# Kernel tuning notes

Hardware: AMD Instinct MI355X
Metric: run time of the kernel (lower is better)

The kernel has to match this reference:

```python
import jax, jax.numpy as jnp
import numpy as np

N = 40962      # icosahedral mesh nodes
E = 245760     # ~degree-6 mesh edges
HD = 256       # hidden_dim
H = 8          # heads
C = HD // H    # out_ch per head = 32
EDIM = 16      # raw edge feature dim
L = 4          # num_layers


def setup_inputs() -> dict:
    key = jax.random.key(0)
    ks = iter(jax.random.split(key, 48))
    def rn(shape, scale=0.05):
        return jax.random.normal(next(ks), shape, dtype=jnp.float32) * scale
    inp = {}
    inp['mesh_enc'] = jax.random.normal(next(ks), (N, HD), dtype=jnp.float32)
    inp['edge_index'] = jax.random.randint(next(ks), (2, E), 0, N)
    inp['edge_attr'] = jax.random.normal(next(ks), (E, EDIM), dtype=jnp.float32)
    # edge input projection
    inp['ep_W'] = rn((EDIM, HD)); inp['ep_b'] = jnp.zeros((HD,), jnp.float32)
    # GATv2 layer 0 (in_ch=HD) and layers 1..L-1 stacked (in_ch=C)
    inp['Wl0'] = rn((HD, H, C));  inp['Wr0'] = rn((HD, H, C))
    inp['Wl'] = rn((L - 1, C, H, C)); inp['Wr'] = rn((L - 1, C, H, C))
    inp['We0'] = rn((HD, H, C));  inp['We'] = rn((L - 1, HD, H, C))
    inp['att0'] = rn((H, C));     inp['att'] = rn((L - 1, H, C))
    inp['Wres0'] = rn((HD, C));   inp['Wres'] = rn((L - 1, C, C))
    inp['bn0'] = jnp.zeros((C,), jnp.float32); inp['bn'] = jnp.zeros((L - 1, C), jnp.float32)
    # edge-update MLP (upd_hidden_dim = hidden_dim * ffn_ratio = HD)
    inp['Wu1_0'] = rn((2 * C + HD, HD)); inp['Wu1'] = rn((L - 1, 2 * C + HD, HD))
    inp['bu1_0'] = jnp.zeros((HD,), jnp.float32); inp['bu1'] = jnp.zeros((L - 1, HD), jnp.float32)
    inp['Wu2_0'] = rn((HD, HD)); inp['Wu2'] = rn((L - 1, HD, HD))
    inp['bu2_0'] = jnp.zeros((HD,), jnp.float32); inp['bu2'] = jnp.zeros((L - 1, HD), jnp.float32)
    # inter-layer LayerNorms (L-1 of them, over C)
    inp['ln_g'] = jnp.ones((L - 1, C), jnp.float32); inp['ln_b'] = jnp.zeros((L - 1, C), jnp.float32)
    # SGFormer-style global branch
    inp['Wq'] = rn((HD, H, C)); inp['Wk'] = rn((HD, H, C)); inp['Wv'] = rn((HD, H, C))
    inp['alpha_p'] = jnp.array(0.5, jnp.float32)
    inp['cn_g'] = jnp.ones((C,), jnp.float32); inp['cn_b'] = jnp.zeros((C,), jnp.float32)
    return inp


def _layernorm(x, g, b):
    mu = x.mean(-1, keepdims=True)
    var = x.var(-1, keepdims=True)
    return (x - mu) / jnp.sqrt(var + 1e-5) * g + b


def _segment_softmax(s, dst, n):
    smax = jax.ops.segment_max(s, dst, num_segments=n)
    smax = jnp.where(jnp.isfinite(smax), smax, 0.0)
    ex = jnp.exp(s - smax[dst])
    den = jax.ops.segment_sum(ex, dst, num_segments=n)
    return ex / (den[dst] + 1e-16)


def _gat(x, e, src, dst, Wl, Wr, We, att, Wres, bn, Wu1, bu1, Wu2, bu2):
    # GATv2 with edge features (PyG semantics), concat=False (head mean), residual
    xl = jnp.einsum('nd,dhc->nhc', x, Wl)          # [N,H,C]
    xr = jnp.einsum('nd,dhc->nhc', x, Wr)
    ee = jnp.einsum('ed,dhc->ehc', e, We)          # [E,H,C]
    m = xl[src] + xr[dst] + ee
    s = jnp.einsum('ehc,hc->eh', jax.nn.leaky_relu(m, 0.2), att)
    a = _segment_softmax(s, dst, x.shape[0])       # [E,H]
    agg = jax.ops.segment_sum(a[:, :, None] * xl[src], dst, num_segments=x.shape[0])
    out = agg.mean(axis=1) + x @ Wres + bn         # [N,C]
    # residual edge update MLP
    h = jnp.concatenate([out[src], out[dst], e], axis=-1)
    e_new = e + jax.nn.gelu(h @ Wu1 + bu1) @ Wu2 + bu2
    return out, e_new


def _sgformer(x, Wq, Wk, Wv):
    # SGFormer linear global attention, O(N)
    q = jnp.einsum('nd,dhc->nhc', x, Wq)
    k = jnp.einsum('nd,dhc->nhc', x, Wk)
    v = jnp.einsum('nd,dhc->nhc', x, Wv)
    qs = q / (jnp.linalg.norm(q, axis=-1, keepdims=True) + 1e-6)
    ks = k / (jnp.linalg.norm(k, axis=-1, keepdims=True) + 1e-6)
    n = jnp.float32(x.shape[0])
    kv = jnp.einsum('nhc,nhd->hcd', ks, v)
    num = jnp.einsum('nhc,hcd->nhd', qs, kv) + n * v
    den = jnp.einsum('nhc,hc->nh', qs, ks.sum(0)) + n
    return (num / den[..., None]).mean(axis=1)     # [N,C]


def reference(mesh_enc, edge_index, edge_attr, ep_W, ep_b, Wl0, Wr0, Wl, Wr, We0, We,
              att0, att, Wres0, Wres, bn0, bn, Wu1_0, Wu1, bu1_0, bu1, Wu2_0, Wu2,
              bu2_0, bu2, ln_g, ln_b, Wq, Wk, Wv, alpha_p, cn_g, cn_b):
    src, dst = edge_index[0], edge_index[1]
    e = edge_attr @ ep_W + ep_b
    x, e = _gat(mesh_enc, e, src, dst, Wl0, Wr0, We0, att0, Wres0, bn0,
                Wu1_0, bu1_0, Wu2_0, bu2_0)
    x = _layernorm(x, ln_g[0], ln_b[0])
    for i in range(L - 1):
        x, e = _gat(x, e, src, dst, Wl[i], Wr[i], We[i], att[i], Wres[i], bn[i],
                    Wu1[i], bu1[i], Wu2[i], bu2[i])
        if i < L - 2:
            x = _layernorm(x, ln_g[i + 1], ln_b[i + 1])
    trans_out = _sgformer(mesh_enc, Wq, Wk, Wv)
    alpha = jax.nn.sigmoid(alpha_p)
    return _layernorm(alpha * x + (1.0 - alpha) * trans_out, cn_g, cn_b)
```

## Files before the change

kernel.cpp:

```cpp
#include <hip/hip_runtime.h>
#include <hip/hip_bf16.h>
#include <math.h>

typedef __hip_bfloat16 bf16;
typedef __attribute__((ext_vector_type(8))) __bf16 bf16x8;
typedef __attribute__((ext_vector_type(4))) float f32x4;

#define NN 40962
#define NE 245760
#define HDIM 256
#define NH 8
#define CH 32

#define MT 64
#define KVB 512

__device__ __forceinline__ float b2f(bf16 v) { return __bfloat162float(v); }
__device__ __forceinline__ bf16 f2b(float v) { return __float2bfloat16(v); }
__device__ __forceinline__ unsigned short f2bs(float v) {
  bf16 b = __float2bfloat16(v);
  return __builtin_bit_cast(unsigned short, b);
}
__device__ __forceinline__ float bs2f(unsigned short u) {
  return __bfloat162float(__builtin_bit_cast(bf16, u));
}

__device__ __forceinline__ float fast_gelu(float x) {
  float x2 = x * x;
  float g = x * (0.7978845608028654f + 0.0356774081f * x2);
  float y = fminf(g * 2.885390081777927f, 60.f);
  float t = exp2f(y);
  float th = (t - 1.f) * __builtin_amdgcn_rcpf(t + 1.f);
  return 0.5f * x * (1.f + th);
}

__global__ __launch_bounds__(512) void k_edge_proj_mfma(
    const float* __restrict__ attr, const unsigned short* __restrict__ Weps,
    const float* __restrict__ bias, bf16* __restrict__ e) {
  __shared__ unsigned short At[MT][40];
  __shared__ unsigned short O[MT][264];
  int tid = threadIdx.x, l = tid & 63, w = tid >> 6;
  int lr = l & 15, lk = l >> 4;
  int base = blockIdx.x * MT;
  {
    int p = tid >> 3, q = tid & 7;
    if (q < 4) {
      float4 v = *reinterpret_cast<const float4*>(&attr[(size_t)(base + p) * 16 + q * 4]);
      unsigned short tmp[4] = {f2bs(v.x), f2bs(v.y), f2bs(v.z), f2bs(v.w)};
      *reinterpret_cast<uint2*>(&At[p][q * 4]) = *reinterpret_cast<const uint2*>(tmp);
    } else {
      unsigned short z[4] = {0, 0, 0, 0};
      *reinterpret_cast<uint2*>(&At[p][q * 4]) = *reinterpret_cast<const uint2*>(z);
    }
  }
  __syncthreads();

  int j0 = w * 32;
  f32x4 acc[4][2];
#pragma unroll
  for (int m = 0; m < 4; ++m)
#pragma unroll
    for (int n = 0; n < 2; ++n)
#pragma unroll
      for (int r = 0; r < 4; ++r) acc[m][n][r] = 0.f;
  {
    bf16x8 a[4], b[2];
#pragma unroll
    for (int m = 0; m < 4; ++m)
      a[m] = *reinterpret_cast<const bf16x8*>(&At[m * 16 + lr][lk * 8]);
#pragma unroll
    for (int n = 0; n < 2; ++n) {
      int nt = w * 2 + n;
      b[n] = *reinterpret_cast<const bf16x8*>(Weps + ((size_t)nt * 64 + l) * 8);
    }
#pragma unroll
    for (int m = 0; m < 4; ++m)
#pragma unroll
      for (int n = 0; n < 2; ++n)
        acc[m][n] = __builtin_amdgcn_mfma_f32_16x16x32_bf16(a[m], b[n], acc[m][n], 0, 0, 0);
  }
#pragma unroll
  for (int n = 0; n < 2; ++n) {
    int col = j0 + n * 16 + lr;
    float bv = bias[col];
#pragma unroll
    for (int m = 0; m < 4; ++m)
#pragma unroll
      for (int r = 0; r < 4; ++r)
        O[m * 16 + lk * 4 + r][col] = f2bs(acc[m][n][r] + bv);
  }
  __syncthreads();
  for (int t = tid; t < MT * 32; t += 512) {
    int p = t >> 5, c = t & 31;
    *reinterpret_cast<uint4*>(&e[(size_t)(base + p) * HDIM + c * 8]) =
        *reinterpret_cast<const uint4*>(&O[p][c * 8]);
  }
}

__global__ void k_csr_count(const int* __restrict__ dst, int* __restrict__ cnt) {
  int e = blockIdx.x * 256 + threadIdx.x;
  if (e < NE) atomicAdd(&cnt[dst[e]], 1);
}
__global__ void k_csr_scan(const int* __restrict__ cnt, int* __restrict__ rowptr,
                           int* __restrict__ cursor) {
  __shared__ int part[256];
  __shared__ int tot;
  int t = threadIdx.x;
  const int CHUNK = (NN + 255) / 256;
  int lo = t * CHUNK, hi = lo + CHUNK; if (hi > NN) hi = NN; if (lo > NN) lo = NN;
  int s = 0;
  for (int i = lo; i < hi; ++i) s += cnt[i];
  part[t] = s;
  __syncthreads();
  if (t == 0) {
    int run = 0;
    for (int i = 0; i < 256; ++i) { int v = part[i]; part[i] = run; run += v; }
    tot = run;
  }
  __syncthreads();
  int run = part[t];
  for (int i = lo; i < hi; ++i) { rowptr[i] = run; cursor[i] = run; run += cnt[i]; }
  if (t == 0) rowptr[NN] = tot;
}
__global__ void k_csr_fill(const int* __restrict__ src, const int* __restrict__ dst,
                           int* __restrict__ cursor, int* __restrict__ csrsrc,
                           int* __restrict__ pos) {
  int e = blockIdx.x * 256 + threadIdx.x;
  if (e >= NE) return;
  int p = atomicAdd(&cursor[dst[e]], 1);
  csrsrc[p] = src[e];
  pos[e] = p;
}

struct SwzP {
  const float *We0, *WeL, *Wl0, *Wr0, *Wq, *Wk, *Wv;
  const float *Wu1_0, *Wu1L, *Wu2_0, *Wu2L, *WlL, *WrL, *epW;
  unsigned short *wall, *w1s, *w2s, *w32s, *wep;
  int* cnt;
};
__device__ __forceinline__ void swz1(const float* __restrict__ W,
                                     unsigned short* __restrict__ out, int t, int Kdiv32) {
  int i = t & 7, l = (t >> 3) & 63;
  int k0 = (t >> 9) % Kdiv32;
  int n0 = t / (512 * Kdiv32);
  int k = k0 * 32 + (l >> 4) * 8 + i;
  int n = n0 * 16 + (l & 15);
  out[t] = f2bs(W[k * 256 + n]);
}
#define SWZ_NW (9 * 65536)
#define SWZ_N1 (3 * 81920)
#define SWZ_N2 (3 * 65536)
#define SWZ_N3 (6 * 8192)
#define SWZ_N4 8192
__global__ void k_swz_fused(SwzP P) {
  int gid = blockIdx.x * 256 + threadIdx.x;
  if (gid < SWZ_NW) {
    int mat = gid >> 16, t = gid & 65535;
    const float* W;
    switch (mat) {
      case 0: W = P.We0; break;
      case 1: W = P.WeL; break;
      case 2: W = P.WeL + 65536; break;
      case 3: W = P.WeL + 131072; break;
      case 4: W = P.Wl0; break;
      case 5: W = P.Wr0; break;
      case 6: W = P.Wq; break;
      case 7: W = P.Wk; break;
      default: W = P.Wv; break;
    }
    swz1(W, P.wall + (size_t)mat * 65536, t, 8);
  } else if (gid < SWZ_NW + SWZ_N1) {
    int idx = gid - SWZ_NW;
    int mat = idx / 81920, t = idx % 81920;
    const float* W = (mat == 0) ? P.Wu1_0 : P.Wu1L + (size_t)(mat - 1) * 81920;
    swz1(W, P.w1s + (size_t)mat * 81920, t, 10);
  } else if (gid < SWZ_NW + SWZ_N1 + SWZ_N2) {
    int idx = gid - SWZ_NW - SWZ_N1;
    int mat = idx >> 16, t = idx & 65535;
    const float* W = (mat == 0) ? P.Wu2_0 : P.Wu2L + (size_t)(mat - 1) * 65536;
    swz1(W, P.w2s + (size_t)mat * 65536, t, 8);
  } else if (gid < SWZ_NW + SWZ_N1 + SWZ_N2 + SWZ_N3) {
    int idx = gid - SWZ_NW - SWZ_N1 - SWZ_N2;
    int mat = idx >> 13, t = idx & 8191;
    int i = mat >> 1;
    const float* W = (mat & 1) ? P.WrL + (size_t)i * 8192 : P.WlL + (size_t)i * 8192;
    swz1(W, P.w32s + (size_t)mat * 8192, t, 1);
  } else if (gid < SWZ_NW + SWZ_N1 + SWZ_N2 + SWZ_N3 + SWZ_N4) {
    int t = gid - (SWZ_NW + SWZ_N1 + SWZ_N2 + SWZ_N3);
    int i = t & 7, l = (t >> 3) & 63;
    int n0 = t >> 9;
    int k = (l >> 4) * 8 + i;
    int n = n0 * 16 + (l & 15);
    P.wep[t] = (k < 16) ? f2bs(P.epW[k * 256 + n]) : (unsigned short)0;
  } else {
    int i = gid - (SWZ_NW + SWZ_N1 + SWZ_N2 + SWZ_N3 + SWZ_N4);
    if (i < NN) P.cnt[i] = 0;
  }
}

__global__ __launch_bounds__(512) void k_edge_score_mfma(
    const bf16* __restrict__ e, const unsigned short* __restrict__ Wes,
    const bf16* __restrict__ xl, const bf16* __restrict__ xr,
    const float* __restrict__ att, const int* __restrict__ src,
    const int* __restrict__ dst, const int* __restrict__ pos,
    float* __restrict__ sxc) {
  __shared__ unsigned short Ae[MT][264];
  __shared__ float attS[HDIM];
  __shared__ int sidx[MT], didx[MT];
  int tid = threadIdx.x, l = tid & 63, w = tid >> 6;
  int lr = l & 15, lk = l >> 4;
  int base = blockIdx.x * MT;
  if (tid < HDIM) attS[tid] = att[tid];
  if (tid < MT) sidx[tid] = src[base + tid];
  else if (tid < 2 * MT) didx[tid - MT] = dst[base + tid - MT];
  for (int t = tid; t < MT * 32; t += 512) {
    int p = t >> 5, c = t & 31;
    *reinterpret_cast<uint4*>(&Ae[p][c * 8]) =
        *reinterpret_cast<const uint4*>(&e[(size_t)(base + p) * HDIM + c * 8]);
  }
  __syncthreads();

  f32x4 acc[4][2];
#pragma unroll
  for (int m = 0; m < 4; ++m)
#pragma unroll
    for (int n = 0; n < 2; ++n)
#pragma unroll
      for (int r = 0; r < 4; ++r) acc[m][n][r] = 0.f;
  for (int k0 = 0; k0 < 8; ++k0) {
    bf16x8 a[4], b[2];
#pragma unroll
    for (int m = 0; m < 4; ++m)
      a[m] = *reinterpret_cast<const bf16x8*>(&Ae[m * 16 + lr][k0 * 32 + lk * 8]);
#pragma unroll
    for (int n = 0; n < 2; ++n) {
      int nt = w * 2 + n;
      b[n] = *reinterpret_cast<const bf16x8*>(Wes + ((size_t)(nt * 8 + k0) * 64 + l) * 8);
    }
#pragma unroll
    for (int m = 0; m < 4; ++m)
#pragma unroll
      for (int n = 0; n < 2; ++n)
        acc[m][n] = __builtin_amdgcn_mfma_f32_16x16x32_bf16(a[m], b[n], acc[m][n], 0, 0, 0);
  }
  __syncthreads();

#pragma unroll
  for (int n = 0; n < 2; ++n) {
    int col = w * 32 + n * 16 + lr;
    float av = attS[col];
#pragma unroll
    for (int m = 0; m < 4; ++m)
#pragma unroll
      for (int r = 0; r < 4; ++r) {
        int row = m * 16 + lk * 4 + r;
        float xs = b2f(xl[(size_t)sidx[row] * HDIM + col]) +
                   b2f(xr[(size_t)didx[row] * HDIM + col]);
        float mm = acc[m][n][r] + xs;
        mm = (mm > 0.f) ? mm : 0.2f * mm;
        Ae[row][col] = f2bs(mm * av);
      }
  }
  __syncthreads();
  for (int pair = tid; pair < MT * NH; pair += 512) {
    int ed = pair >> 3, h = pair & 7;
    float s = 0.f;
#pragma unroll
    for (int c = 0; c < CH; ++c) s += bs2f(Ae[ed][h * CH + c]);
    sxc[(size_t)pos[base + ed] * NH + h] = expf(s);
  }
}

#define GCHUNK 64
template <int ID, bool LN>
__global__ __launch_bounds__(256) void k_gat_out(
    const int* __restrict__ rowptr, const int* __restrict__ csrsrc,
    const float* __restrict__ sxc, const bf16* __restrict__ xl,
    const float* __restrict__ x, const float* __restrict__ Wres,
    const float* __restrict__ bn, const float* __restrict__ lng,
    const float* __restrict__ lnb, float* __restrict__ xpre,
    float* __restrict__ xpost) {
  int n = blockIdx.x;
  int j = threadIdx.x;
  int h = j >> 5, c = j & 31;
  int p0 = rowptr[n], p1 = rowptr[n + 1];
  __shared__ int srcS[GCHUNK];
  __shared__ float exS[GCHUNK * NH];
  float a = 0.f, dsum = 0.f;
  for (int pb = p0; pb < p1; pb += GCHUNK) {
    int chunk = p1 - pb; if (chunk > GCHUNK) chunk = GCHUNK;
    if (j < chunk) srcS[j] = csrsrc[pb + j];
    for (int t = j; t < chunk * NH; t += 256) exS[t] = sxc[(size_t)pb * NH + t];
    __syncthreads();
    int i = 0;
    for (; i + 4 <= chunk; i += 4) {
      float e0 = exS[(i + 0) * NH + h], e1 = exS[(i + 1) * NH + h];
      float e2 = exS[(i + 2) * NH + h], e3 = exS[(i + 3) * NH + h];
      float x0 = b2f(xl[(size_t)srcS[i + 0] * HDIM + j]);
      float x1 = b2f(xl[(size_t)srcS[i + 1] * HDIM + j]);
      float x2 = b2f(xl[(size_t)srcS[i + 2] * HDIM + j]);
      float x3 = b2f(xl[(size_t)srcS[i + 3] * HDIM + j]);
      a += e0 * x0 + e1 * x1 + e2 * x2 + e3 * x3;
      dsum += e0 + e1 + e2 + e3;
    }
    for (; i < chunk; ++i) {
      float ev = exS[i * NH + h];
      a += ev * b2f(xl[(size_t)srcS[i] * HDIM + j]);
      dsum += ev;
    }
    __syncthreads();
  }
  __shared__ float oh[HDIM];
  __shared__ float rs[NH][CH];
  __shared__ float oc[CH + 1];
  oh[j] = a / (dsum + 1e-16f);
  const int KS = ID / NH;
  float r = 0.f;
  for (int k = h * KS; k < (h + 1) * KS; ++k)
    r += x[(size_t)n * ID + k] * Wres[k * CH + c];
  rs[h][c] = r;
  __syncthreads();
  if (j < CH) {
    float o = 0.f;
#pragma unroll
    for (int hh = 0; hh < NH; ++hh) o += oh[hh * CH + j];
    o *= (1.f / NH);
    float rr = 0.f;
#pragma unroll
    for (int hh = 0; hh < NH; ++hh) rr += rs[hh][j];
    o += rr + bn[j];
    xpre[(size_t)n * CH + j] = o;
    oc[j] = o;
  }
  __syncthreads();
  if (LN && j < CH) {
    float mu = 0.f;
#pragma unroll
    for (int k = 0; k < CH; ++k) mu += oc[k];
    mu *= (1.f / CH);
    float var = 0.f;
#pragma unroll
    for (int k = 0; k < CH; ++k) { float d = oc[k] - mu; var += d * d; }
    var *= (1.f / CH);
    xpost[(size_t)n * CH + j] = (oc[j] - mu) * rsqrtf(var + 1e-5f) * lng[j] + lnb[j];
  }
}

__global__ __launch_bounds__(512) void k_edge_mlp_mfma(
    bf16* __restrict__ e, const float* __restrict__ xo,
    const int* __restrict__ src, const int* __restrict__ dst,
    const unsigned short* __restrict__ W1s, const float* __restrict__ bu1,
    const unsigned short* __restrict__ W2s, const float* __restrict__ bu2) {
  __shared__ unsigned short buf[MT][328];
  __shared__ int sidx[MT], didx[MT];
  int tid = threadIdx.x;
  int l = tid & 63;
  int w = tid >> 6;
  int base = blockIdx.x * MT;
  int lr = l & 15;
  int lk = l >> 4;

  if (tid < MT) sidx[tid] = src[base + tid];
  else if (tid < 2 * MT) didx[tid - MT] = dst[base + tid - MT];
  __syncthreads();

  for (int t = tid; t < MT * 32; t += 512) {
    int p = t >> 5, cc = t & 31;
    uint4 v = *reinterpret_cast<const uint4*>(&e[(size_t)(base + p) * HDIM + cc * 8]);
    *reinterpret_cast<uint4*>(&buf[p][64 + cc * 8]) = v;
  }
  for (int t = tid; t < MT * 64; t += 512) {
    int p = t >> 6, c = t & 63;
    float v = (c < CH) ? xo[(size_t)sidx[p] * CH + c]
                       : xo[(size_t)didx[p] * CH + (c - CH)];
    buf[p][c] = f2bs(v);
  }
  __syncthreads();

  int j0 = w * 32;

  f32x4 acc[4][2];
#pragma unroll
  for (int m = 0; m < 4; ++m)
#pragma unroll
    for (int n = 0; n < 2; ++n)
#pragma unroll
      for (int r = 0; r < 4; ++r) acc[m][n][r] = 0.f;

  for (int k0 = 0; k0 < 10; ++k0) {
    bf16x8 a[4], b[2];
#pragma unroll
    for (int m = 0; m < 4; ++m)
      a[m] = *reinterpret_cast<const bf16x8*>(&buf[m * 16 + lr][k0 * 32 + lk * 8]);
#pragma unroll
    for (int n = 0; n < 2; ++n) {
      int nt = w * 2 + n;
      b[n] = *reinterpret_cast<const bf16x8*>(W1s + ((size_t)(nt * 10 + k0) * 64 + l) * 8);
    }
#pragma unroll
    for (int m = 0; m < 4; ++m)
#pragma unroll
      for (int n = 0; n < 2; ++n)
        acc[m][n] = __builtin_amdgcn_mfma_f32_16x16x32_bf16(a[m], b[n], acc[m][n], 0, 0, 0);
  }
  __syncthreads();

#pragma unroll
  for (int n = 0; n < 2; ++n) {
    float bv = bu1[j0 + n * 16 + lr];
#pragma unroll
    for (int m = 0; m < 4; ++m)
#pragma unroll
      for (int r = 0; r < 4; ++r) {
        float g = fast_gelu(acc[m][n][r] + bv);
        buf[m * 16 + lk * 4 + r][j0 + n * 16 + lr] = f2bs(g);
      }
  }
  __syncthreads();

#pragma unroll
  for (int m = 0; m < 4; ++m)
#pragma unroll
    for (int n = 0; n < 2; ++n)
#pragma unroll
      for (int r = 0; r < 4; ++r) acc[m][n][r] = 0.f;

  for (int k0 = 0; k0 < 8; ++k0) {
    bf16x8 a[4], b[2];
#pragma unroll
    for (int m = 0; m < 4; ++m)
      a[m] = *reinterpret_cast<const bf16x8*>(&buf[m * 16 + lr][k0 * 32 + lk * 8]);
#pragma unroll
    for (int n = 0; n < 2; ++n) {
      int nt = w * 2 + n;
      b[n] = *reinterpret_cast<const bf16x8*>(W2s + ((size_t)(nt * 8 + k0) * 64 + l) * 8);
    }
#pragma unroll
    for (int m = 0; m < 4; ++m)
#pragma unroll
      for (int n = 0; n < 2; ++n)
        acc[m][n] = __builtin_amdgcn_mfma_f32_16x16x32_bf16(a[m], b[n], acc[m][n], 0, 0, 0);
  }
  __syncthreads();

#pragma unroll
  for (int n = 0; n < 2; ++n) {
    int col = j0 + n * 16 + lr;
    float bv = bu2[col];
#pragma unroll
    for (int m = 0; m < 4; ++m)
#pragma unroll
      for (int r = 0; r < 4; ++r)
        buf[m * 16 + lk * 4 + r][col] = f2bs(acc[m][n][r] + bv);
  }
  __syncthreads();

  for (int t = tid; t < MT * 32; t += 512) {
    int p = t >> 5, cc = t & 31;
    uint4 dv = *reinterpret_cast<const uint4*>(&buf[p][cc * 8]);
    uint4 ev = *reinterpret_cast<const uint4*>(&e[(size_t)(base + p) * HDIM + cc * 8]);
    const unsigned short* dd = (const unsigned short*)&dv;
    const unsigned short* ee = (const unsigned short*)&ev;
    unsigned short ov[8];
#pragma unroll
    for (int i = 0; i < 8; ++i) ov[i] = f2bs(bs2f(ee[i]) + bs2f(dd[i]));
    *reinterpret_cast<uint4*>(&e[(size_t)(base + p) * HDIM + cc * 8]) =
        *reinterpret_cast<const uint4*>(ov);
  }
}

__global__ __launch_bounds__(256) void k_node_proj0_mfma(
    const float* __restrict__ x, const unsigned short* __restrict__ Wls,
    const unsigned short* __restrict__ Wrs, bf16* __restrict__ xl,
    bf16* __restrict__ xr) {
  __shared__ unsigned short A[MT][264];
  __shared__ unsigned short O[MT][264];
  int tid = threadIdx.x, l = tid & 63, w = tid >> 6;
  int lr = l & 15, lk = l >> 4;
  int base = blockIdx.x * MT;
  for (int t = tid; t < MT * 64; t += 256) {
    int p = t >> 6, c = t & 63;
    int row = base + p; if (row >= NN) row = NN - 1;
    float4 v = *reinterpret_cast<const float4*>(&x[(size_t)row * HDIM + c * 4]);
    unsigned short tmp[4] = {f2bs(v.x), f2bs(v.y), f2bs(v.z), f2bs(v.w)};
    *reinterpret_cast<uint2*>(&A[p][c * 4]) = *reinterpret_cast<const uint2*>(tmp);
  }
  __syncthreads();
  int j0 = w * 64;
#pragma unroll
  for (int mtx = 0; mtx < 2; ++mtx) {
    const unsigned short* Ws = (mtx == 0) ? Wls : Wrs;
    bf16* outp = (mtx == 0) ? xl : xr;
    f32x4 acc[4][4];
#pragma unroll
    for (int m = 0; m < 4; ++m)
#pragma unroll
      for (int n = 0; n < 4; ++n)
#pragma unroll
        for (int r = 0; r < 4; ++r) acc[m][n][r] = 0.f;
    for (int k0 = 0; k0 < 8; ++k0) {
      bf16x8 a[4], b[4];
#pragma unroll
      for (int m = 0; m < 4; ++m)
        a[m] = *reinterpret_cast<const bf16x8*>(&A[m * 16 + lr][k0 * 32 + lk * 8]);
#pragma unroll
      for (int n = 0; n < 4; ++n) {
        int nt = (j0 >> 4) + n;
        b[n] = *reinterpret_cast<const bf16x8*>(Ws + ((size_t)(nt * 8 + k0) * 64 + l) * 8);
      }
#pragma unroll
      for (int m = 0; m < 4; ++m)
#pragma unroll
        for (int n = 0; n < 4; ++n)
          acc[m][n] = __builtin_amdgcn_mfma_f32_16x16x32_bf16(a[m], b[n], acc[m][n], 0, 0, 0);
    }
#pragma unroll
    for (int n = 0; n < 4; ++n)
#pragma unroll
      for (int m = 0; m < 4; ++m)
#pragma unroll
        for (int r = 0; r < 4; ++r)
          O[m * 16 + lk * 4 + r][j0 + n * 16 + lr] = f2bs(acc[m][n][r]);
    __syncthreads();
    for (int t = tid; t < MT * 32; t += 256) {
      int p = t >> 5, c = t & 31;
      if (base + p < NN)
        *reinterpret_cast<uint4*>(&outp[(size_t)(base + p) * HDIM + c * 8]) =
            *reinterpret_cast<const uint4*>(&O[p][c * 8]);
    }
    __syncthreads();
  }
}

__global__ __launch_bounds__(256) void k_node_projS_mfma(
    const float* __restrict__ x, const unsigned short* __restrict__ Wls,
    const unsigned short* __restrict__ Wrs, bf16* __restrict__ xl,
    bf16* __restrict__ xr) {
  __shared__ unsigned short A[MT][40];
  __shared__ unsigned short O[MT][264];
  int tid = threadIdx.x, l = tid & 63, w = tid >> 6;
  int lr = l & 15, lk = l >> 4;
  int base = blockIdx.x * MT;
  for (int t = tid; t < MT * 8; t += 256) {
    int p = t >> 3, q = t & 7;
    int row = base + p; if (row >= NN) row = NN - 1;
    float4 v = *reinterpret_cast<const float4*>(&x[(size_t)row * CH + q * 4]);
    unsigned short tmp[4] = {f2bs(v.x), f2bs(v.y), f2bs(v.z), f2bs(v.w)};
    *reinterpret_cast<uint2*>(&A[p][q * 4]) = *reinterpret_cast<const uint2*>(tmp);
  }
  __syncthreads();
  int j0 = w * 64;
#pragma unroll
  for (int mtx = 0; mtx < 2; ++mtx) {
    const unsigned short* Ws = (mtx == 0) ? Wls : Wrs;
    bf16* outp = (mtx == 0) ? xl : xr;
    f32x4 acc[4][4];
#pragma unroll
    for (int m = 0; m < 4; ++m)
#pragma unroll
      for (int n = 0; n < 4; ++n)
#pragma unroll
        for (int r = 0; r < 4; ++r) acc[m][n][r] = 0.f;
    bf16x8 a[4], b[4];
#pragma unroll
    for (int m = 0; m < 4; ++m)
      a[m] = *reinterpret_cast<const bf16x8*>(&A[m * 16 + lr][lk * 8]);
#pragma unroll
    for (int n = 0; n < 4; ++n) {
      int nt = (j0 >> 4) + n;
      b[n] = *reinterpret_cast<const bf16x8*>(Ws + ((size_t)nt * 64 + l) * 8);
    }
#pragma unroll
    for (int m = 0; m < 4; ++m)
#pragma unroll
      for (int n = 0; n < 4; ++n)
        acc[m][n] = __builtin_amdgcn_mfma_f32_16x16x32_bf16(a[m], b[n], acc[m][n], 0, 0, 0);
#pragma unroll
    for (int n = 0; n < 4; ++n)
#pragma unroll
      for (int m = 0; m < 4; ++m)
#pragma unroll
        for (int r = 0; r < 4; ++r)
          O[m * 16 + lk * 4 + r][j0 + n * 16 + lr] = f2bs(acc[m][n][r]);
    __syncthreads();
    for (int t = tid; t < MT * 32; t += 256) {
      int p = t >> 5, c = t & 31;
      if (base + p < NN)
        *reinterpret_cast<uint4*>(&outp[(size_t)(base + p) * HDIM + c * 8]) =
            *reinterpret_cast<const uint4*>(&O[p][c * 8]);
    }
    __syncthreads();
  }
}

__global__ __launch_bounds__(256) void k_sg_qkv_mfma(
    const float* __restrict__ x, const unsigned short* __restrict__ Wqs,
    const unsigned short* __restrict__ Wks, const unsigned short* __restrict__ Wvs,
    bf16* __restrict__ qs, bf16* __restrict__ ks, bf16* __restrict__ vv) {
  __shared__ unsigned short A[MT][264];
  __shared__ unsigned short O[MT][264];
  int tid = threadIdx.x, l = tid & 63, w = tid >> 6;
  int lr = l & 15, lk = l >> 4;
  int base = blockIdx.x * MT;
  for (int t = tid; t < MT * 64; t += 256) {
    int p = t >> 6, c = t & 63;
    int row = base + p; if (row >= NN) row = NN - 1;
    float4 v = *reinterpret_cast<const float4*>(&x[(size_t)row * HDIM + c * 4]);
    unsigned short tmp[4] = {f2bs(v.x), f2bs(v.y), f2bs(v.z), f2bs(v.w)};
    *reinterpret_cast<uint2*>(&A[p][c * 4]) = *reinterpret_cast<const uint2*>(tmp);
  }
  __syncthreads();
  int j0 = w * 64;
#pragma unroll
  for (int mtx = 0; mtx < 3; ++mtx) {
    const unsigned short* Ws = (mtx == 0) ? Wqs : (mtx == 1) ? Wks : Wvs;
    bf16* outp = (mtx == 0) ? qs : (mtx == 1) ? ks : vv;
    f32x4 acc[4][4];
#pragma unroll
    for (int m = 0; m < 4; ++m)
#pragma unroll
      for (int n = 0; n < 4; ++n)
#pragma unroll
        for (int r = 0; r < 4; ++r) acc[m][n][r] = 0.f;
    for (int k0 = 0; k0 < 8; ++k0) {
      bf16x8 a[4], b[4];
#pragma unroll
      for (int m = 0; m < 4; ++m)
        a[m] = *reinterpret_cast<const bf16x8*>(&A[m * 16 + lr][k0 * 32 + lk * 8]);
#pragma unroll
      for (int n = 0; n < 4; ++n) {
        int nt = (j0 >> 4) + n;
        b[n] = *reinterpret_cast<const bf16x8*>(Ws + ((size_t)(nt * 8 + k0) * 64 + l) * 8);
      }
#pragma unroll
      for (int m = 0; m < 4; ++m)
#pragma unroll
        for (int n = 0; n < 4; ++n)
          acc[m][n] = __builtin_amdgcn_mfma_f32_16x16x32_bf16(a[m], b[n], acc[m][n], 0, 0, 0);
    }
    if (mtx < 2) {
      float pa[4][4], pb[4][4];
#pragma unroll
      for (int m = 0; m < 4; ++m)
#pragma unroll
        for (int r = 0; r < 4; ++r) {
          pa[m][r] = acc[m][0][r] * acc[m][0][r] + acc[m][1][r] * acc[m][1][r];
          pb[m][r] = acc[m][2][r] * acc[m][2][r] + acc[m][3][r] * acc[m][3][r];
        }
#pragma unroll
      for (int off = 1; off < 16; off <<= 1) {
#pragma unroll
        for (int m = 0; m < 4; ++m)
#pragma unroll
          for (int r = 0; r < 4; ++r) {
            pa[m][r] += __shfl_xor(pa[m][r], off);
            pb[m][r] += __shfl_xor(pb[m][r], off);
          }
      }
#pragma unroll
      for (int m = 0; m < 4; ++m)
#pragma unroll
        for (int r = 0; r < 4; ++r) {
          float ra = 1.f / (sqrtf(pa[m][r]) + 1e-6f);
          float rb = 1.f / (sqrtf(pb[m][r]) + 1e-6f);
          acc[m][0][r] *= ra; acc[m][1][r] *= ra;
          acc[m][2][r] *= rb; acc[m][3][r] *= rb;
        }
    }
#pragma unroll
    for (int n = 0; n < 4; ++n)
#pragma unroll
      for (int m = 0; m < 4; ++m)
#pragma unroll
        for (int r = 0; r < 4; ++r)
          O[m * 16 + lk * 4 + r][j0 + n * 16 + lr] = f2bs(acc[m][n][r]);
    __syncthreads();
    for (int t = tid; t < MT * 32; t += 256) {
      int p = t >> 5, c = t & 31;
      if (base + p < NN)
        *reinterpret_cast<uint4*>(&outp[(size_t)(base + p) * HDIM + c * 8]) =
            *reinterpret_cast<const uint4*>(&O[p][c * 8]);
    }
    __syncthreads();
  }
}

__global__ void k_sg_kv1(const bf16* __restrict__ ks, const bf16* __restrict__ vv,
                         float* __restrict__ part) {
  int t = threadIdx.x;
  int h = t >> 5;
  float kvloc[CH];
  float ksl = 0.f;
#pragma unroll
  for (int d = 0; d < CH; ++d) kvloc[d] = 0.f;
  __shared__ float krow[HDIM], vrow[HDIM];
  for (int n = blockIdx.x; n < NN; n += KVB) {
    krow[t] = b2f(ks[(size_t)n * HDIM + t]);
    vrow[t] = b2f(vv[(size_t)n * HDIM + t]);
    __syncthreads();
    float kc = krow[t];
    ksl += kc;
#pragma unroll
    for (int d = 0; d < CH; ++d) kvloc[d] += kc * vrow[h * CH + d];
    __syncthreads();
  }
  float* dstp = part + (size_t)blockIdx.x * 8448;
#pragma unroll
  for (int d = 0; d < CH; d += 4)
    *reinterpret_cast<float4*>(&dstp[t * CH + d]) =
        *reinterpret_cast<const float4*>(&kvloc[d]);
  dstp[8192 + t] = ksl;
}

__global__ void k_sg_kv2(const float* __restrict__ part, float* __restrict__ kv,
                         float* __restrict__ ksum) {
  int idx = blockIdx.x * 256 + threadIdx.x;
  if (idx >= 8448) return;
  float s = 0.f;
  for (int b = 0; b < KVB; ++b) s += part[(size_t)b * 8448 + idx];
  if (idx < 8192) kv[idx] = s;
  else ksum[idx - 8192] = s;
}

__global__ void k_sg_final(const bf16* __restrict__ qs, const bf16* __restrict__ vv,
                           const float* __restrict__ kv, const float* __restrict__ ksum,
                           const float* __restrict__ xg, const float* __restrict__ alphap,
                           const float* __restrict__ cng, const float* __restrict__ cnb,
                           float* __restrict__ out) {
  int t = threadIdx.x;
  int d = t & 31, sub = t >> 5;
  __shared__ float qrow[8][HDIM];
  __shared__ float crow[8][CH];
  int n = blockIdx.x * 8 + sub;
  for (int tt = t; tt < 8 * HDIM; tt += 256) {
    int p = tt >> 8, k = tt & 255;
    int n2 = blockIdx.x * 8 + p;
    if (n2 < NN) qrow[p][k] = b2f(qs[(size_t)n2 * HDIM + k]);
  }
  __syncthreads();
  float alpha = 1.f / (1.f + expf(-alphap[0]));
  const float Nf = (float)NN;
  float comb = 0.f;
  if (n < NN) {
    float acc = 0.f;
#pragma unroll
    for (int h = 0; h < NH; ++h) {
      float nm = 0.f, dp = 0.f;
#pragma unroll 8
      for (int c = 0; c < CH; ++c) {
        float qv = qrow[sub][h * CH + c];
        nm += qv * kv[(h * CH + c) * CH + d];
        dp += qv * ksum[h * CH + c];
      }
      nm += Nf * b2f(vv[(size_t)n * HDIM + h * CH + d]);
      acc += nm / (dp + Nf);
    }
    float trans = acc * (1.f / NH);
    comb = alpha * xg[(size_t)n * CH + d] + (1.f - alpha) * trans;
    crow[sub][d] = comb;
  }
  __syncthreads();
  if (n < NN) {
    float mu = 0.f;
#pragma unroll
    for (int k = 0; k < CH; ++k) mu += crow[sub][k];
    mu *= (1.f / CH);
    float var = 0.f;
#pragma unroll
    for (int k = 0; k < CH; ++k) { float dv = crow[sub][k] - mu; var += dv * dv; }
    var *= (1.f / CH);
    float o = (comb - mu) * rsqrtf(var + 1e-5f) * cng[d] + cnb[d];
    out[(size_t)n * CH + d] = o;
  }
}

extern "C" void kernel_launch(void* const* d_in, const int* in_sizes, int n_in,
                              void* d_out, int out_size, void* d_ws, size_t ws_size,
                              hipStream_t stream) {
  const float* mesh  = (const float*)d_in[0];
  const int*   eidx  = (const int*)d_in[1];
  const float* eattr = (const float*)d_in[2];
  const float* epW   = (const float*)d_in[3];
  const float* epb   = (const float*)d_in[4];
  const float* Wl0   = (const float*)d_in[5];
  const float* Wr0   = (const float*)d_in[6];
  const float* WlL   = (const float*)d_in[7];
  const float* WrL   = (const float*)d_in[8];
  const float* We0   = (const float*)d_in[9];
  const float* WeL   = (const float*)d_in[10];
  const float* att0  = (const float*)d_in[11];
  const float* attL  = (const float*)d_in[12];
  const float* Wres0 = (const float*)d_in[13];
  const float* WresL = (const float*)d_in[14];
  const float* bn0   = (const float*)d_in[15];
  const float* bnL   = (const float*)d_in[16];
  const float* Wu1_0 = (const float*)d_in[17];
  const float* Wu1L  = (const float*)d_in[18];
  const float* bu1_0 = (const float*)d_in[19];
  const float* bu1L  = (const float*)d_in[20];
  const float* Wu2_0 = (const float*)d_in[21];
  const float* Wu2L  = (const float*)d_in[22];
  const float* bu2_0 = (const float*)d_in[23];
  const float* bu2L  = (const float*)d_in[24];
  const float* lng   = (const float*)d_in[25];
  const float* lnb   = (const float*)d_in[26];
  const float* Wq    = (const float*)d_in[27];
  const float* Wk    = (const float*)d_in[28];
  const float* Wv    = (const float*)d_in[29];
  const float* alphap= (const float*)d_in[30];
  const float* cng   = (const float*)d_in[31];
  const float* cnb   = (const float*)d_in[32];

  const int* src = eidx;
  const int* dst = eidx + NE;

  char* base = (char*)d_ws;
  size_t o = 0;
  auto alloc = [&](size_t bytes) -> char* {
    o = (o + 255) & ~(size_t)255;
    char* p = base + o;
    o += bytes;
    return p;
  };
  bf16* e    = (bf16*)alloc((size_t)NE * HDIM * 2);
  bf16* xl   = (bf16*)alloc((size_t)NN * HDIM * 2);
  bf16* xr   = (bf16*)alloc((size_t)NN * HDIM * 2);
  bf16* vvb  = (bf16*)alloc((size_t)NN * HDIM * 2);
  float* sxc = (float*)alloc((size_t)NE * NH * 4);
  float* xa  = (float*)alloc((size_t)NN * CH * 4);
  float* xb  = (float*)alloc((size_t)NN * CH * 4);
  float* xc  = (float*)alloc((size_t)NN * CH * 4);
  float* kv  = (float*)alloc(NH * CH * CH * 4);
  float* ksum= (float*)alloc(NH * CH * 4);
  float* kvpart = (float*)alloc((size_t)KVB * 8448 * 4);
  unsigned short* w1s = (unsigned short*)alloc((size_t)3 * 320 * 256 * 2);
  unsigned short* w2s = (unsigned short*)alloc((size_t)3 * 256 * 256 * 2);
  unsigned short* wall= (unsigned short*)alloc((size_t)9 * 65536 * 2);
  unsigned short* w32s= (unsigned short*)alloc((size_t)6 * 32 * 256 * 2);
  unsigned short* wep = (unsigned short*)alloc((size_t)SWZ_N4 * 2);
  int* cnt    = (int*)alloc((size_t)NN * 4);
  int* rowptr = (int*)alloc((size_t)(NN + 1) * 4);
  int* cursor = (int*)alloc((size_t)NN * 4);
  int* csrsrc = (int*)alloc((size_t)NE * 4);
  int* pos    = (int*)alloc((size_t)NE * 4);
  if (ws_size < o) return;

  SwzP P;
  P.We0 = We0; P.WeL = WeL; P.Wl0 = Wl0; P.Wr0 = Wr0; P.Wq = Wq; P.Wk = Wk; P.Wv = Wv;
  P.Wu1_0 = Wu1_0; P.Wu1L = Wu1L; P.Wu2_0 = Wu2_0; P.Wu2L = Wu2L;
  P.WlL = WlL; P.WrL = WrL; P.epW = epW;
  P.wall = wall; P.w1s = w1s; P.w2s = w2s; P.w32s = w32s; P.wep = wep; P.cnt = cnt;
  int swz_total = SWZ_NW + SWZ_N1 + SWZ_N2 + SWZ_N3 + SWZ_N4 + NN;
  k_swz_fused<<<(swz_total + 255) / 256, 256, 0, stream>>>(P);

  k_csr_count<<<(NE + 255) / 256, 256, 0, stream>>>(dst, cnt);
  k_csr_scan<<<1, 256, 0, stream>>>(cnt, rowptr, cursor);
  k_csr_fill<<<(NE + 255) / 256, 256, 0, stream>>>(src, dst, cursor, csrsrc, pos);

  k_edge_proj_mfma<<<NE / MT, 512, 0, stream>>>(eattr, wep, epb, e);

  const float* xin = mesh;
  float* post = xb;
  for (int l = 0; l < 4; ++l) {
    const float *att_p, *Wres_p, *bn_p, *bu1_p, *bu2_p;
    if (l == 0) {
      att_p = att0; Wres_p = Wres0; bn_p = bn0; bu1_p = bu1_0; bu2_p = bu2_0;
    } else {
      int i = l - 1;
      att_p = attL + (size_t)i * HDIM;
      Wres_p = WresL + (size_t)i * CH * CH;
      bn_p = bnL + (size_t)i * CH;
      bu1_p = bu1L + (size_t)i * HDIM;
      bu2_p = bu2L + (size_t)i * HDIM;
    }

    if (l == 0)
      k_node_proj0_mfma<<<(NN + MT - 1) / MT, 256, 0, stream>>>(
          mesh, wall + (size_t)4 * 65536, wall + (size_t)5 * 65536, xl, xr);
    else
      k_node_projS_mfma<<<(NN + MT - 1) / MT, 256, 0, stream>>>(
          xin, w32s + (size_t)((l - 1) * 2 + 0) * 8192,
          w32s + (size_t)((l - 1) * 2 + 1) * 8192, xl, xr);

    k_edge_score_mfma<<<NE / MT, 512, 0, stream>>>(e, wall + (size_t)l * 65536,
                                                   xl, xr, att_p, src, dst, pos, sxc);

    if (l == 0)
      k_gat_out<HDIM, true><<<NN, 256, 0, stream>>>(rowptr, csrsrc, sxc, xl, xin, Wres_p,
                                                    bn_p, lng, lnb, xa, post);
    else if (l < 3)
      k_gat_out<CH, true><<<NN, 256, 0, stream>>>(rowptr, csrsrc, sxc, xl, xin, Wres_p,
                                                  bn_p, lng + (size_t)l * CH,
                                                  lnb + (size_t)l * CH, xa, post);
    else
      k_gat_out<CH, false><<<NN, 256, 0, stream>>>(rowptr, csrsrc, sxc, xl, xin, Wres_p,
                                                   bn_p, nullptr, nullptr, xa, nullptr);

    if (l < 3)
      k_edge_mlp_mfma<<<NE / MT, 512, 0, stream>>>(e, xa, src, dst,
                                                   w1s + (size_t)l * 320 * 256, bu1_p,
                                                   w2s + (size_t)l * 256 * 256, bu2_p);

    xin = post;
    post = (post == xb) ? xc : xb;
  }

  k_sg_qkv_mfma<<<(NN + MT - 1) / MT, 256, 0, stream>>>(
      mesh, wall + (size_t)6 * 65536, wall + (size_t)7 * 65536,
      wall + (size_t)8 * 65536, xl, xr, vvb);
  k_sg_kv1<<<KVB, 256, 0, stream>>>(xr, vvb, kvpart);
  k_sg_kv2<<<33, 256, 0, stream>>>(kvpart, kv, ksum);
  k_sg_final<<<(NN + 7) / 8, 256, 0, stream>>>(xl, vvb, kv, ksum, xa, alphap, cng, cnb,
                                               (float*)d_out);
}
```

Measured before the change: 1.426 ms.

## Store edges in CSR order and fuse next-layer edge scoring into edge MLP

Edges are permuted into destination-sorted CSR order at projection time, so edge features, scores and src/dst indices are all addressed by CSR position. This removes the pos scatter and keeps gather locality. The next layer's node projection now runs before the edge MLP, and the MLP kernel computes that layer's attention scores from the freshly updated edge tile while it is still in shared memory. This avoids a separate pass that re-reads the full edge tensor for scoring, at the cost of a heavier fused kernel with more registers and shared memory.

```diff
diff --git a/kernel.cpp b/kernel.cpp
--- a/kernel.cpp
+++ b/kernel.cpp
@@ -35,17 +35,21 @@
 }
 
 __global__ __launch_bounds__(512) void k_edge_proj_mfma(
-    const float* __restrict__ attr, const unsigned short* __restrict__ Weps,
-    const float* __restrict__ bias, bf16* __restrict__ e) {
+    const float* __restrict__ attr, const int* __restrict__ csre,
+    const unsigned short* __restrict__ Weps, const float* __restrict__ bias,
+    bf16* __restrict__ e) {
   __shared__ unsigned short At[MT][40];
   __shared__ unsigned short O[MT][264];
+  __shared__ int ceS[MT];
   int tid = threadIdx.x, l = tid & 63, w = tid >> 6;
   int lr = l & 15, lk = l >> 4;
   int base = blockIdx.x * MT;
+  if (tid < MT) ceS[tid] = csre[base + tid];
+  __syncthreads();
   {
     int p = tid >> 3, q = tid & 7;
     if (q < 4) {
-      float4 v = *reinterpret_cast<const float4*>(&attr[(size_t)(base + p) * 16 + q * 4]);
+      float4 v = *reinterpret_cast<const float4*>(&attr[(size_t)ceS[p] * 16 + q * 4]);
       unsigned short tmp[4] = {f2bs(v.x), f2bs(v.y), f2bs(v.z), f2bs(v.w)};
       *reinterpret_cast<uint2*>(&At[p][q * 4]) = *reinterpret_cast<const uint2*>(tmp);
     } else {
@@ -123,13 +127,14 @@
   if (t == 0) rowptr[NN] = tot;
 }
 __global__ void k_csr_fill(const int* __restrict__ src, const int* __restrict__ dst,
-                           int* __restrict__ cursor, int* __restrict__ csrsrc,
-                           int* __restrict__ pos) {
+                           int* __restrict__ cursor, int* __restrict__ csre,
+                           int* __restrict__ psrc, int* __restrict__ pdst) {
   int e = blockIdx.x * 256 + threadIdx.x;
   if (e >= NE) return;
   int p = atomicAdd(&cursor[dst[e]], 1);
-  csrsrc[p] = src[e];
-  pos[e] = p;
+  csre[p] = e;
+  psrc[p] = src[e];
+  pdst[p] = dst[e];
 }
 
 struct SwzP {
@@ -201,9 +206,8 @@
 __global__ __launch_bounds__(512) void k_edge_score_mfma(
     const bf16* __restrict__ e, const unsigned short* __restrict__ Wes,
     const bf16* __restrict__ xl, const bf16* __restrict__ xr,
-    const float* __restrict__ att, const int* __restrict__ src,
-    const int* __restrict__ dst, const int* __restrict__ pos,
-    float* __restrict__ sxc) {
+    const float* __restrict__ att, const int* __restrict__ psrc,
+    const int* __restrict__ pdst, float* __restrict__ sxc) {
   __shared__ unsigned short Ae[MT][264];
   __shared__ float attS[HDIM];
   __shared__ int sidx[MT], didx[MT];
@@ -211,8 +215,8 @@
   int lr = l & 15, lk = l >> 4;
   int base = blockIdx.x * MT;
   if (tid < HDIM) attS[tid] = att[tid];
-  if (tid < MT) sidx[tid] = src[base + tid];
-  else if (tid < 2 * MT) didx[tid - MT] = dst[base + tid - MT];
+  if (tid < MT) sidx[tid] = psrc[base + tid];
+  else if (tid < 2 * MT) didx[tid - MT] = pdst[base + tid - MT];
   for (int t = tid; t < MT * 32; t += 512) {
     int p = t >> 5, c = t & 31;
     *reinterpret_cast<uint4*>(&Ae[p][c * 8]) =
@@ -267,14 +271,14 @@
     float s = 0.f;
 #pragma unroll
     for (int c = 0; c < CH; ++c) s += bs2f(Ae[ed][h * CH + c]);
-    sxc[(size_t)pos[base + ed] * NH + h] = expf(s);
+    sxc[(size_t)(base + ed) * NH + h] = expf(s);
   }
 }
 
 #define GCHUNK 64
 template <int ID, bool LN>
 __global__ __launch_bounds__(256) void k_gat_out(
-    const int* __restrict__ rowptr, const int* __restrict__ csrsrc,
+    const int* __restrict__ rowptr, const int* __restrict__ psrc,
     const float* __restrict__ sxc, const bf16* __restrict__ xl,
     const float* __restrict__ x, const float* __restrict__ Wres,
     const float* __restrict__ bn, const float* __restrict__ lng,
@@ -289,7 +293,7 @@
   float a = 0.f, dsum = 0.f;
   for (int pb = p0; pb < p1; pb += GCHUNK) {
     int chunk = p1 - pb; if (chunk > GCHUNK) chunk = GCHUNK;
-    if (j < chunk) srcS[j] = csrsrc[pb + j];
+    if (j < chunk) srcS[j] = psrc[pb + j];
     for (int t = j; t < chunk * NH; t += 256) exS[t] = sxc[(size_t)pb * NH + t];
     __syncthreads();
     int i = 0;
@@ -346,12 +350,16 @@
   }
 }
 
-__global__ __launch_bounds__(512) void k_edge_mlp_mfma(
+__global__ __launch_bounds__(512) void k_edge_mlp_fused(
     bf16* __restrict__ e, const float* __restrict__ xo,
-    const int* __restrict__ src, const int* __restrict__ dst,
+    const int* __restrict__ psrc, const int* __restrict__ pdst,
     const unsigned short* __restrict__ W1s, const float* __restrict__ bu1,
-    const unsigned short* __restrict__ W2s, const float* __restrict__ bu2) {
+    const unsigned short* __restrict__ W2s, const float* __restrict__ bu2,
+    const unsigned short* __restrict__ Wes2, const float* __restrict__ att2,
+    const bf16* __restrict__ xl2, const bf16* __restrict__ xr2,
+    float* __restrict__ sxc) {
   __shared__ unsigned short buf[MT][328];
+  __shared__ float attS[HDIM];
   __shared__ int sidx[MT], didx[MT];
   int tid = threadIdx.x;
   int l = tid & 63;
@@ -360,8 +368,9 @@
   int lr = l & 15;
   int lk = l >> 4;
 
-  if (tid < MT) sidx[tid] = src[base + tid];
-  else if (tid < 2 * MT) didx[tid - MT] = dst[base + tid - MT];
+  if (tid < HDIM) attS[tid] = att2[tid];
+  if (tid < MT) sidx[tid] = psrc[base + tid];
+  else if (tid < 2 * MT) didx[tid - MT] = pdst[base + tid - MT];
   __syncthreads();
 
   for (int t = tid; t < MT * 32; t += 512) {
@@ -466,6 +475,57 @@
     for (int i = 0; i < 8; ++i) ov[i] = f2bs(bs2f(ee[i]) + bs2f(dd[i]));
     *reinterpret_cast<uint4*>(&e[(size_t)(base + p) * HDIM + cc * 8]) =
         *reinterpret_cast<const uint4*>(ov);
+    *reinterpret_cast<uint4*>(&buf[p][cc * 8]) = *reinterpret_cast<const uint4*>(ov);
+  }
+  __syncthreads();
+
+#pragma unroll
+  for (int m = 0; m < 4; ++m)
+#pragma unroll
+    for (int n = 0; n < 2; ++n)
+#pragma unroll
+      for (int r = 0; r < 4; ++r) acc[m][n][r] = 0.f;
+  for (int k0 = 0; k0 < 8; ++k0) {
+    bf16x8 a[4], b[2];
+#pragma unroll
+    for (int m = 0; m < 4; ++m)
+      a[m] = *reinterpret_cast<const bf16x8*>(&buf[m * 16 + lr][k0 * 32 + lk * 8]);
+#pragma unroll
+    for (int n = 0; n < 2; ++n) {
+      int nt = w * 2 + n;
+      b[n] = *reinterpret_cast<const bf16x8*>(Wes2 + ((size_t)(nt * 8 + k0) * 64 + l) * 8);
+    }
+#pragma unroll
+    for (int m = 0; m < 4; ++m)
+#pragma unroll
+      for (int n = 0; n < 2; ++n)
+        acc[m][n] = __builtin_amdgcn_mfma_f32_16x16x32_bf16(a[m], b[n], acc[m][n], 0, 0, 0);
+  }
+  __syncthreads();
+
+#pragma unroll
+  for (int n = 0; n < 2; ++n) {
+    int col = j0 + n * 16 + lr;
+    float av = attS[col];
+#pragma unroll
+    for (int m = 0; m < 4; ++m)
+#pragma unroll
+      for (int r = 0; r < 4; ++r) {
+        int row = m * 16 + lk * 4 + r;
+        float xs = b2f(xl2[(size_t)sidx[row] * HDIM + col]) +
+                   b2f(xr2[(size_t)didx[row] * HDIM + col]);
+        float mm = acc[m][n][r] + xs;
+        mm = (mm > 0.f) ? mm : 0.2f * mm;
+        buf[row][col] = f2bs(mm * av);
+      }
+  }
+  __syncthreads();
+  for (int pair = tid; pair < MT * NH; pair += 512) {
+    int ed = pair >> 3, h = pair & 7;
+    float s = 0.f;
+#pragma unroll
+    for (int c = 0; c < CH; ++c) s += bs2f(buf[ed][h * CH + c]);
+    sxc[(size_t)(base + ed) * NH + h] = expf(s);
   }
 }
 
@@ -841,8 +901,9 @@
   int* cnt    = (int*)alloc((size_t)NN * 4);
   int* rowptr = (int*)alloc((size_t)(NN + 1) * 4);
   int* cursor = (int*)alloc((size_t)NN * 4);
-  int* csrsrc = (int*)alloc((size_t)NE * 4);
-  int* pos    = (int*)alloc((size_t)NE * 4);
+  int* csre   = (int*)alloc((size_t)NE * 4);
+  int* psrc   = (int*)alloc((size_t)NE * 4);
+  int* pdst   = (int*)alloc((size_t)NE * 4);
   if (ws_size < o) return;
 
   SwzP P;
@@ -855,51 +916,49 @@
 
   k_csr_count<<<(NE + 255) / 256, 256, 0, stream>>>(dst, cnt);
   k_csr_scan<<<1, 256, 0, stream>>>(cnt, rowptr, cursor);
-  k_csr_fill<<<(NE + 255) / 256, 256, 0, stream>>>(src, dst, cursor, csrsrc, pos);
-
-  k_edge_proj_mfma<<<NE / MT, 512, 0, stream>>>(eattr, wep, epb, e);
+  k_csr_fill<<<(NE + 255) / 256, 256, 0, stream>>>(src, dst, cursor, csre, psrc, pdst);
+
+  k_edge_proj_mfma<<<NE / MT, 512, 0, stream>>>(eattr, csre, wep, epb, e);
 
   const float* xin = mesh;
   float* post = xb;
   for (int l = 0; l < 4; ++l) {
-    const float *att_p, *Wres_p, *bn_p, *bu1_p, *bu2_p;
+    const float *Wres_p, *bn_p;
+    if (l == 0) { Wres_p = Wres0; bn_p = bn0; }
+    else {
+      Wres_p = WresL + (size_t)(l - 1) * CH * CH;
+      bn_p = bnL + (size_t)(l - 1) * CH;
+    }
+
     if (l == 0) {
-      att_p = att0; Wres_p = Wres0; bn_p = bn0; bu1_p = bu1_0; bu2_p = bu2_0;
-    } else {
-      int i = l - 1;
-      att_p = attL + (size_t)i * HDIM;
-      Wres_p = WresL + (size_t)i * CH * CH;
-      bn_p = bnL + (size_t)i * CH;
-      bu1_p = bu1L + (size_t)i * HDIM;
-      bu2_p = bu2L + (size_t)i * HDIM;
-    }
-
-    if (l == 0)
       k_node_proj0_mfma<<<(NN + MT - 1) / MT, 256, 0, stream>>>(
           mesh, wall + (size_t)4 * 65536, wall + (size_t)5 * 65536, xl, xr);
-    else
-      k_node_projS_mfma<<<(NN + MT - 1) / MT, 256, 0, stream>>>(
-          xin, w32s + (size_t)((l - 1) * 2 + 0) * 8192,
-          w32s + (size_t)((l - 1) * 2 + 1) * 8192, xl, xr);
-
-    k_edge_score_mfma<<<NE / MT, 512, 0, stream>>>(e, wall + (size_t)l * 65536,
-                                                   xl, xr, att_p, src, dst, pos, sxc);
+      k_edge_score_mfma<<<NE / MT, 512, 0, stream>>>(e, wall, xl, xr, att0,
+                                                     psrc, pdst, sxc);
+    }
 
     if (l == 0)
-      k_gat_out<HDIM, true><<<NN, 256, 0, stream>>>(rowptr, csrsrc, sxc, xl, xin, Wres_p,
+      k_gat_out<HDIM, true><<<NN, 256, 0, stream>>>(rowptr, psrc, sxc, xl, xin, Wres_p,
                                                     bn_p, lng, lnb, xa, post);
     else if (l < 3)
-      k_gat_out<CH, true><<<NN, 256, 0, stream>>>(rowptr, csrsrc, sxc, xl, xin, Wres_p,
+      k_gat_out<CH, true><<<NN, 256, 0, stream>>>(rowptr, psrc, sxc, xl, xin, Wres_p,
                                                   bn_p, lng + (size_t)l * CH,
                                                   lnb + (size_t)l * CH, xa, post);
     else
-      k_gat_out<CH, false><<<NN, 256, 0, stream>>>(rowptr, csrsrc, sxc, xl, xin, Wres_p,
+      k_gat_out<CH, false><<<NN, 256, 0, stream>>>(rowptr, psrc, sxc, xl, xin, Wres_p,
                                                    bn_p, nullptr, nullptr, xa, nullptr);
 
-    if (l < 3)
-      k_edge_mlp_mfma<<<NE / MT, 512, 0, stream>>>(e, xa, src, dst,
-                                                   w1s + (size_t)l * 320 * 256, bu1_p,
-                                                   w2s + (size_t)l * 256 * 256, bu2_p);
+    if (l < 3) {
+      k_node_projS_mfma<<<(NN + MT - 1) / MT, 256, 0, stream>>>(
+          post, w32s + (size_t)(l * 2 + 0) * 8192,
+          w32s + (size_t)(l * 2 + 1) * 8192, xl, xr);
+      k_edge_mlp_fused<<<NE / MT, 512, 0, stream>>>(
+          e, xa, psrc, pdst,
+          w1s + (size_t)l * 320 * 256, (l == 0) ? bu1_0 : bu1L + (size_t)(l - 1) * HDIM,
+          w2s + (size_t)l * 256 * 256, (l == 0) ? bu2_0 : bu2L + (size_t)(l - 1) * HDIM,
+          wall + (size_t)(l + 1) * 65536, attL + (size_t)l * HDIM,
+          xl, xr, sxc);
+    }
 
     xin = post;
     post = (post == xb) ? xc : xb;
```

Result: slower. 1.459 ms (+2.3%).
